# Performance work log

Hardware: AMD Instinct MI355X
Metric: run time of the kernel (lower is better)

The kernel has to match this reference:

```python
import jax, jax.numpy as jnp
import numpy as np

T = 32        # time_step
H = 64        # n_hidden (and dense width)
A = 8         # nb_actions
OBS_DIM = 512
B = 4096      # sequences; obs rows = B*T
LN_EPS = 1e-12  # tf.contrib.layers.layer_norm epsilon


def setup_inputs() -> dict:
    key = jax.random.key(0)
    ks = jax.random.split(key, 10)
    s = 0.1
    return {
        "obs":  jax.random.normal(ks[0], (B * T, OBS_DIM), jnp.float32),
        "W0":   jax.random.normal(ks[1], (OBS_DIM, H), jnp.float32) * s,
        "b0":   jnp.zeros((H,), jnp.float32),
        "gamma": jnp.ones((H,), jnp.float32),
        "beta":  jnp.zeros((H,), jnp.float32),
        "Wfw":  jax.random.normal(ks[2], (2 * H, 4 * H), jnp.float32) * s,
        "bfw":  jnp.zeros((4 * H,), jnp.float32),
        "Wbw":  jax.random.normal(ks[3], (2 * H, 4 * H), jnp.float32) * s,
        "bbw":  jnp.zeros((4 * H,), jnp.float32),
        "Wc":   jax.random.uniform(ks[4], (H, A), jnp.float32, -0.003, 0.003),
        "bc":   jnp.zeros((A,), jnp.float32),
    }


def _lstm_scan(xs, W, b):
    """BasicLSTMCell (forget_bias=1.0). xs: [T, B, H] -> hs: [T, B, H]."""
    nb = xs.shape[1]
    init = (jnp.zeros((nb, H), xs.dtype), jnp.zeros((nb, H), xs.dtype))

    def step(carry, x_t):
        c, h = carry
        z = jnp.concatenate([x_t, h], axis=-1) @ W + b  # [B, 4H]
        i, j, f, o = jnp.split(z, 4, axis=-1)           # TF gate order i,j,f,o
        c = c * jax.nn.sigmoid(f + 1.0) + jax.nn.sigmoid(i) * jnp.tanh(j)
        h = jnp.tanh(c) * jax.nn.sigmoid(o)
        return (c, h), h

    _, hs = jax.lax.scan(step, init, xs)
    return hs


def reference(obs, W0, b0, gamma, beta, Wfw, bfw, Wbw, bbw, Wc, bc):
    # dense(64) + layer_norm + relu
    x = obs @ W0 + b0                                   # [B*T, H]
    mu = jnp.mean(x, axis=-1, keepdims=True)
    var = jnp.mean(jnp.square(x - mu), axis=-1, keepdims=True)
    x = gamma * (x - mu) / jnp.sqrt(var + LN_EPS) + beta
    x = jax.nn.relu(x)

    xt = x.reshape(-1, T, H).transpose(1, 0, 2)          # [T, B, H]
    hs_fw = _lstm_scan(xt, Wfw, bfw)                     # [T, B, H]
    hs_bw = _lstm_scan(xt[::-1], Wbw, bbw)[::-1]         # reverse-in, reverse-out

    # tf.reshape on the (fw, bw) tuple stacks along a new leading axis:
    # [2, B, T, H] -> [2B, T*H, 1]; conv1d(kernel=stride=H) == per-step proj.
    y = jnp.stack([hs_fw.transpose(1, 0, 2), hs_bw.transpose(1, 0, 2)], axis=0)
    y = y.reshape(-1, T, H)                              # [2B, T, H]
    out = jnp.tanh(jnp.einsum('btk,ka->bta', y, Wc) + bc)  # [2B, T, A]
    return out
```

## Files before the change

### kernel.cpp

```cpp
#include <hip/hip_runtime.h>
#include <hip/hip_bf16.h>

typedef __attribute__((ext_vector_type(8))) short bf16x8;
typedef __attribute__((ext_vector_type(4))) float f32x4;

#define MFMA_BF16 __builtin_amdgcn_mfma_f32_16x16x32_bf16

#define GLDS16(gp, lp)                                                        \
  __builtin_amdgcn_global_load_lds(                                           \
      (const __attribute__((address_space(1))) void*)(gp),                    \
      (__attribute__((address_space(3))) void*)(lp), 16, 0, 0)

__device__ __forceinline__ unsigned pk2(float a, float b) {
  __hip_bfloat162 t = __float22bfloat162_rn(make_float2(a, b));
  return *reinterpret_cast<unsigned*>(&t);
}
__device__ __forceinline__ unsigned short f2bf_hw(float f) {
  __hip_bfloat16 h = __float2bfloat16(f);
  return *reinterpret_cast<unsigned short*>(&h);
}

__global__ void k0_conv(const float* __restrict__ W0, const float* __restrict__ Wfw,
                        const float* __restrict__ Wbw, unsigned short* __restrict__ wfrag,
                        unsigned short* __restrict__ wlstm) {
  int gid = blockIdx.x * 256 + threadIdx.x;
  if (gid < 4096) {
    int f = gid >> 6, l = gid & 63;
    int k0 = (f >> 2) * 32 + ((l >> 4) << 3);
    int n = (f & 3) * 16 + (l & 15);
    bf16x8 v;
#pragma unroll
    for (int j = 0; j < 8; ++j) v[j] = (short)f2bf_hw(W0[(k0 + j) * 64 + n]);
    *(bf16x8*)(wfrag + gid * 8) = v;
  } else if (gid < 12288) {
    int g2 = gid - 4096;
    const float* W = (g2 < 4096) ? Wfw : Wbw;
    int f = (g2 & 4095) >> 6, l = g2 & 63;
    int wv = f >> 4, gate = (f >> 2) & 3, kf = f & 3;
    int col = gate * 64 + wv * 16 + (l & 15);
    int kr = kf * 32 + ((l >> 4) << 3);
    bf16x8 v;
#pragma unroll
    for (int j = 0; j < 8; ++j) v[j] = (short)f2bf_hw(W[(kr + j) * 256 + col]);
    *(bf16x8*)(wlstm + g2 * 8) = v;
  }
}

__global__ __launch_bounds__(256, 3) void k_dense_ln(
    const float* __restrict__ obs, const unsigned short* __restrict__ wfrag,
    const float* __restrict__ b0, const float* __restrict__ gam,
    const float* __restrict__ bet, unsigned short* __restrict__ xout) {
  __shared__ __align__(16) char lds[49152];
  const int tid = threadIdx.x, w = tid >> 6, l = tid & 63;
  const int g = l >> 4, c = l & 15;
  const long blk64 = (long)blockIdx.x * 64;
  const long rb = blk64 + w * 16;

  float b0v[4], gv[4], bv[4];
#pragma unroll
  for (int nt = 0; nt < 4; ++nt) {
    int col = nt * 16 + c;
    b0v[nt] = b0[col]; gv[nt] = gam[col]; bv[nt] = bet[col];
  }
  const unsigned short* wfl = wfrag + l * 8;
  const char* gB = (const char*)obs + blk64 * 2048;

  const int rlo = w * 4 + g;
  asm volatile("s_waitcnt vmcnt(0)" ::: "memory");

#define K1_STAGE(q)                                                           \
  {                                                                           \
    _Pragma("unroll") for (int i = 0; i < 4; ++i) {                           \
      int row_ = i * 16 + rlo;                                                \
      const char* gp_ = gB + (long)row_ * 2048 + (q) * 256 +                  \
                        (long)((c ^ rlo) * 16);                               \
      char* lp_ = lds + ((q) % 3) * 16384 + (i * 4096 + (w * 64 + l) * 16);   \
      GLDS16(gp_, lp_);                                                       \
    }                                                                         \
  }

  K1_STAGE(0);
  K1_STAGE(1);
  K1_STAGE(2);

  f32x4 acc[4];
#pragma unroll
  for (int nt = 0; nt < 4; ++nt) acc[nt] = (f32x4){0.f, 0.f, 0.f, 0.f};

#pragma unroll
  for (int q = 0; q < 8; ++q) {
    constexpr int VW[8] = {8, 16, 24, 24, 24, 24, 20, 16};
    asm volatile("s_waitcnt vmcnt(%0)" :: "i"(VW[q]) : "memory");
    __builtin_amdgcn_s_barrier();
    __builtin_amdgcn_sched_barrier(0);

    const char* rowb = lds + (q % 3) * 16384 + (w * 16 + c) * 256;
#pragma unroll
    for (int kf = 0; kf < 2; ++kf) {
      int fb = (q * 2 + kf) * 4;
      bf16x8 B0 = *(const bf16x8*)(wfl + (fb + 0) * 512);
      bf16x8 B1 = *(const bf16x8*)(wfl + (fb + 1) * 512);
      bf16x8 B2 = *(const bf16x8*)(wfl + (fb + 2) * 512);
      bf16x8 B3 = *(const bf16x8*)(wfl + (fb + 3) * 512);
      int u0 = kf * 8 + g * 2;
      float4 f0 = *(const float4*)(rowb + ((u0 + 0) ^ c) * 16);
      float4 f1 = *(const float4*)(rowb + ((u0 + 1) ^ c) * 16);
      union { bf16x8 v; unsigned u[4]; } af;
      af.u[0] = pk2(f0.x, f0.y); af.u[1] = pk2(f0.z, f0.w);
      af.u[2] = pk2(f1.x, f1.y); af.u[3] = pk2(f1.z, f1.w);
      acc[0] = MFMA_BF16(af.v, B0, acc[0], 0, 0, 0);
      acc[1] = MFMA_BF16(af.v, B1, acc[1], 0, 0, 0);
      acc[2] = MFMA_BF16(af.v, B2, acc[2], 0, 0, 0);
      acc[3] = MFMA_BF16(af.v, B3, acc[3], 0, 0, 0);
    }
    if (q < 5) {
      __builtin_amdgcn_s_barrier();
      __builtin_amdgcn_sched_barrier(0);
      K1_STAGE(q + 3);
    }
  }

  float vv[4][4], s1[4], s2[4];
#pragma unroll
  for (int r = 0; r < 4; ++r) { s1[r] = 0.f; s2[r] = 0.f; }
#pragma unroll
  for (int nt = 0; nt < 4; ++nt)
#pragma unroll
    for (int r = 0; r < 4; ++r) {
      float val = acc[nt][r] + b0v[nt];
      vv[nt][r] = val; s1[r] += val; s2[r] += val * val;
    }
#pragma unroll
  for (int r = 0; r < 4; ++r) {
#pragma unroll
    for (int m = 1; m <= 8; m <<= 1) {
      s1[r] += __shfl_xor(s1[r], m);
      s2[r] += __shfl_xor(s2[r], m);
    }
  }
  unsigned short* xw = (unsigned short*)lds + w * 1024;
#pragma unroll
  for (int r = 0; r < 4; ++r) {
    float mu = s1[r] * 0.015625f;
    float var = s2[r] * 0.015625f - mu * mu;
    float inv = rsqrtf(var + 1e-12f);
    int row = g * 4 + r;
#pragma unroll
    for (int nt = 0; nt < 4; ++nt) {
      float xn = (vv[nt][r] - mu) * inv * gv[nt] + bv[nt];
      xw[(row * 64 + nt * 16 + c) ^ (g << 3)] = f2bf_hw(fmaxf(xn, 0.f));
    }
  }
#pragma unroll
  for (int m2 = 0; m2 < 2; ++m2) {
    int m = m2 * 64 + l;
    int row = m >> 3, u8 = m & 7;
    bf16x8 v = *(const bf16x8*)(xw + ((row * 64 + u8 * 8) ^ ((row >> 2) << 3)));
    *(bf16x8*)(xout + (rb + row) * 64 + u8 * 8) = v;
  }
}

__global__ __launch_bounds__(256, 2) void k_lstm(
    const unsigned short* __restrict__ x, const unsigned short* __restrict__ wlstm,
    const float* __restrict__ bfw, const float* __restrict__ bbw,
    const float* __restrict__ Wc, const float* __restrict__ bc,
    float* __restrict__ out) {
  __shared__ __align__(16) char xl[65536];
  __shared__ unsigned short hl[2 * 1024];
  const int tid = threadIdx.x, w = tid >> 6, l = tid & 63;
  const int g = l >> 4, c = l & 15;
  const int dir = blockIdx.x >> 8;
  const int sq = (blockIdx.x & 255) * 16;
  const float* bias = dir ? bbw : bfw;

  bf16x8 Bf[4][4];
  const unsigned short* wl = wlstm + ((long)dir * 4096 + w * 16 * 64) * 8;
#pragma unroll
  for (int gate = 0; gate < 4; ++gate)
#pragma unroll
    for (int kf = 0; kf < 4; ++kf)
      Bf[gate][kf] = *(const bf16x8*)(wl + ((gate * 4 + kf) * 64 + l) * 8);
  float bz[4];
#pragma unroll
  for (int gate = 0; gate < 4; ++gate) bz[gate] = bias[gate * 64 + w * 16 + c];

  bf16x8 Pc[2];
#pragma unroll
  for (int kf = 0; kf < 2; ++kf)
#pragma unroll
    for (int j = 0; j < 8; ++j) Pc[kf][j] = 0;
  float bcv = 0.f;
  if (w == 0 && c < 8) {
#pragma unroll
    for (int kf = 0; kf < 2; ++kf)
#pragma unroll
      for (int j = 0; j < 8; ++j)
        Pc[kf][j] = (short)f2bf_hw(Wc[(kf * 32 + g * 8 + j) * 8 + c]);
    bcv = bc[c];
  }

  asm volatile("s_waitcnt vmcnt(0)" ::: "memory");

  const int ss = l >> 3, sc = l & 7;
#pragma unroll
  for (int j = 0; j < 8; ++j) {
    int tt = w * 8 + j;
    int te = dir ? 31 - tt : tt;
#pragma unroll
    for (int p = 0; p < 2; ++p) {
      int s = p * 8 + ss;
      const char* gp = (const char*)x +
          ((long)(sq + s) * 32 + te) * 128 + (long)(sc ^ (s & 7)) * 16;
      char* lp = xl + tt * 2048 + p * 1024;
      GLDS16(gp, lp);
    }
  }

  for (int i = tid; i < 1024; i += 256) ((unsigned*)hl)[i] = 0u;
  float cs[4] = {0.f, 0.f, 0.f, 0.f};

  if (w == 0) asm volatile("s_waitcnt vmcnt(12)" ::: "memory");
  asm volatile("s_waitcnt lgkmcnt(0)" ::: "memory");
  __builtin_amdgcn_s_barrier();
  __builtin_amdgcn_sched_barrier(0);

  const int hq = w >> 1;
  const int hgp = ((w & 1) * 2 + (c >> 3)) * 16;
  const int hlo = c & 7;

  f32x4 accx[4];
  {
    const char* xt = xl + 0 * 2048 + c * 128;
    bf16x8 Ax0 = *(const bf16x8*)(xt + (long)((g) ^ (c & 7)) * 16);
    bf16x8 Ax1 = *(const bf16x8*)(xt + (long)((4 + g) ^ (c & 7)) * 16);
#pragma unroll
    for (int gate = 0; gate < 4; ++gate) {
      f32x4 b = (f32x4){bz[gate], bz[gate], bz[gate], bz[gate]};
      accx[gate] = MFMA_BF16(Ax1, Bf[gate][1],
                             MFMA_BF16(Ax0, Bf[gate][0], b, 0, 0, 0), 0, 0, 0);
    }
  }

  int p = 0;
#pragma unroll
  for (int t = 0; t < 32; ++t) {
    bf16x8 Ah0 = *(const bf16x8*)((const char*)hl + p * 2048 + l * 16);
    bf16x8 Ah1 = *(const bf16x8*)((const char*)hl + p * 2048 + 1024 + l * 16);

    f32x4 acc[4];
#pragma unroll
    for (int gate = 0; gate < 4; ++gate)
      acc[gate] = MFMA_BF16(Ah1, Bf[gate][3],
                            MFMA_BF16(Ah0, Bf[gate][2], accx[gate], 0, 0, 0),
                            0, 0, 0);

    if (t + 1 < 32) {
      const char* xt = xl + (t + 1) * 2048 + c * 128;
      bf16x8 Ax0 = *(const bf16x8*)(xt + (long)((g) ^ (c & 7)) * 16);
      bf16x8 Ax1 = *(const bf16x8*)(xt + (long)((4 + g) ^ (c & 7)) * 16);
#pragma unroll
      for (int gate = 0; gate < 4; ++gate) {
        f32x4 b = (f32x4){bz[gate], bz[gate], bz[gate], bz[gate]};
        accx[gate] = MFMA_BF16(Ax1, Bf[gate][1],
                               MFMA_BF16(Ax0, Bf[gate][0], b, 0, 0, 0), 0, 0, 0);
      }
    }

    const int wb = (p ^ 1) * 1024;
#pragma unroll
    for (int r = 0; r < 4; ++r) {
      float ei = __expf(-acc[0][r]);
      float ej = __expf(2.f * acc[1][r]);
      float ef = __expf(-(acc[2][r] + 1.f));
      float eo = __expf(-acc[3][r]);
      float p12 = (1.f + ei) * (1.f + ej);
      float r3 = __builtin_amdgcn_rcpf(p12 * (1.f + ef));
      float it = (ej - 1.f) * (1.f + ef) * r3;
      float sf = p12 * r3;
      cs[r] = cs[r] * sf + it;
      float ec = __expf(2.f * cs[r]);
      float r2 = __builtin_amdgcn_rcpf((1.f + eo) * (1.f + ec));
      hl[wb + (hq * 64 + hgp + 4 * g + r) * 8 + hlo] =
          f2bf_hw((ec - 1.f) * r2);
    }

    if (t + 2 < 32) {
      if (w == ((t + 2) >> 3))
        asm volatile("s_waitcnt vmcnt(%0)" :: "i"(14 - 2 * ((t + 2) & 7)) : "memory");
    }
    asm volatile("s_waitcnt lgkmcnt(0)" ::: "memory");
    __builtin_amdgcn_s_barrier();
    __builtin_amdgcn_sched_barrier(0);

    if (w == 0 && t >= 1) {
      int te = dir ? 31 - t : t;
      f32x4 pa = (f32x4){0.f, 0.f, 0.f, 0.f};
      pa = MFMA_BF16(Ah0, Pc[0], pa, 0, 0, 0);
      pa = MFMA_BF16(Ah1, Pc[1], pa, 0, 0, 0);
      if (c < 8) {
        int tp = dir ? 32 - t : t - 1;
#pragma unroll
        for (int r = 0; r < 4; ++r) {
          long orow = (long)dir * 4096 + sq + 4 * g + r;
          out[(orow * 32 + tp) * 8 + c] = tanhf(pa[r] + bcv);
        }
      }
    }
    p ^= 1;
  }

  if (w == 0) {
    bf16x8 Ph0 = *(const bf16x8*)((const char*)hl + p * 2048 + l * 16);
    bf16x8 Ph1 = *(const bf16x8*)((const char*)hl + p * 2048 + 1024 + l * 16);
    f32x4 pa = (f32x4){0.f, 0.f, 0.f, 0.f};
    pa = MFMA_BF16(Ph0, Pc[0], pa, 0, 0, 0);
    pa = MFMA_BF16(Ph1, Pc[1], pa, 0, 0, 0);
    if (c < 8) {
      int tp = dir ? 0 : 31;
#pragma unroll
      for (int r = 0; r < 4; ++r) {
        long orow = (long)dir * 4096 + sq + 4 * g + r;
        out[(orow * 32 + tp) * 8 + c] = tanhf(pa[r] + bcv);
      }
    }
  }
}

extern "C" void kernel_launch(void* const* d_in, const int* in_sizes, int n_in,
                              void* d_out, int out_size, void* d_ws, size_t ws_size,
                              hipStream_t stream) {
  const float* obs = (const float*)d_in[0];
  const float* W0  = (const float*)d_in[1];
  const float* b0  = (const float*)d_in[2];
  const float* gam = (const float*)d_in[3];
  const float* bet = (const float*)d_in[4];
  const float* Wfw = (const float*)d_in[5];
  const float* bfw = (const float*)d_in[6];
  const float* Wbw = (const float*)d_in[7];
  const float* bbw = (const float*)d_in[8];
  const float* Wc  = (const float*)d_in[9];
  const float* bc  = (const float*)d_in[10];
  float* out = (float*)d_out;

  unsigned short* wfrag = (unsigned short*)d_ws;
  unsigned short* wlstm = wfrag + 4096 * 8;
  unsigned short* xbf   = wlstm + 8192 * 8;

  k0_conv<<<48, 256, 0, stream>>>(W0, Wfw, Wbw, wfrag, wlstm);
  k_dense_ln<<<2048, 256, 0, stream>>>(obs, wfrag, b0, gam, bet, xbf);
  k_lstm<<<512, 256, 0, stream>>>(xbf, wlstm, bfw, bbw, Wc, bc, out);
}
```

Measured before the change: 102.3 us.

## Restructure dense-LN loading and spread LSTM output projection across waves

The dense+layernorm kernel now uses 128-thread blocks where each wave loads its entire 16-row obs tile into a private 32KB LDS region up front, instead of running a 3-stage block-wide pipeline with barriers. The MFMA loop double-buffers the weight fragments in registers. In the LSTM kernel, the per-timestep output projection is split across all four waves, replacing the previous wave-0-only work. Staggered vmcnt waits are replaced by a single full wait, partial unrolling is used, and tanhf is replaced with an exp/rcp form. The trade-off is that loads no longer overlap compute within a wave, the LSTM kernel has a longer startup stall, and tanh precision is slightly lower.

```diff
diff --git a/kernel.cpp b/kernel.cpp
--- a/kernel.cpp
+++ b/kernel.cpp
@@ -18,6 +18,9 @@
 __device__ __forceinline__ unsigned short f2bf_hw(float f) {
   __hip_bfloat16 h = __float2bfloat16(f);
   return *reinterpret_cast<unsigned short*>(&h);
+}
+__device__ __forceinline__ float tanh_f(float x) {
+  return 1.f - 2.f * __builtin_amdgcn_rcpf(1.f + __expf(2.f * x));
 }
 
 __global__ void k0_conv(const float* __restrict__ W0, const float* __restrict__ Wfw,
@@ -46,15 +49,15 @@
   }
 }
 
-__global__ __launch_bounds__(256, 3) void k_dense_ln(
+__global__ __launch_bounds__(128) void k_dense_ln(
     const float* __restrict__ obs, const unsigned short* __restrict__ wfrag,
     const float* __restrict__ b0, const float* __restrict__ gam,
     const float* __restrict__ bet, unsigned short* __restrict__ xout) {
-  __shared__ __align__(16) char lds[49152];
+  __shared__ __align__(16) char lds[65536];
   const int tid = threadIdx.x, w = tid >> 6, l = tid & 63;
   const int g = l >> 4, c = l & 15;
-  const long blk64 = (long)blockIdx.x * 64;
-  const long rb = blk64 + w * 16;
+  const long rw = (long)blockIdx.x * 32 + w * 16;
+  char* ldw = lds + w * 32768;
 
   float b0v[4], gv[4], bv[4];
 #pragma unroll
@@ -63,60 +66,50 @@
     b0v[nt] = b0[col]; gv[nt] = gam[col]; bv[nt] = bet[col];
   }
   const unsigned short* wfl = wfrag + l * 8;
-  const char* gB = (const char*)obs + blk64 * 2048;
-
-  const int rlo = w * 4 + g;
+  const char* gW = (const char*)obs + rw * 2048;
+
   asm volatile("s_waitcnt vmcnt(0)" ::: "memory");
 
-#define K1_STAGE(q)                                                           \
-  {                                                                           \
-    _Pragma("unroll") for (int i = 0; i < 4; ++i) {                           \
-      int row_ = i * 16 + rlo;                                                \
-      const char* gp_ = gB + (long)row_ * 2048 + (q) * 256 +                  \
-                        (long)((c ^ rlo) * 16);                               \
-      char* lp_ = lds + ((q) % 3) * 16384 + (i * 4096 + (w * 64 + l) * 16);   \
-      GLDS16(gp_, lp_);                                                       \
-    }                                                                         \
-  }
-
-  K1_STAGE(0);
-  K1_STAGE(1);
-  K1_STAGE(2);
+#pragma unroll
+  for (int i = 0; i < 32; ++i) {
+    int ri = i >> 1, hi = i & 1;
+    const char* gp = gW + ri * 2048 + hi * 1024 + (long)((l ^ (ri & 7)) * 16);
+    char* lp = ldw + ri * 2048 + hi * 1024;
+    GLDS16(gp, lp);
+  }
+  asm volatile("s_waitcnt vmcnt(0)" ::: "memory");
+  __builtin_amdgcn_sched_barrier(0);
 
   f32x4 acc[4];
 #pragma unroll
   for (int nt = 0; nt < 4; ++nt) acc[nt] = (f32x4){0.f, 0.f, 0.f, 0.f};
 
-#pragma unroll
-  for (int q = 0; q < 8; ++q) {
-    constexpr int VW[8] = {8, 16, 24, 24, 24, 24, 20, 16};
-    asm volatile("s_waitcnt vmcnt(%0)" :: "i"(VW[q]) : "memory");
-    __builtin_amdgcn_s_barrier();
-    __builtin_amdgcn_sched_barrier(0);
-
-    const char* rowb = lds + (q % 3) * 16384 + (w * 16 + c) * 256;
-#pragma unroll
-    for (int kf = 0; kf < 2; ++kf) {
-      int fb = (q * 2 + kf) * 4;
-      bf16x8 B0 = *(const bf16x8*)(wfl + (fb + 0) * 512);
-      bf16x8 B1 = *(const bf16x8*)(wfl + (fb + 1) * 512);
-      bf16x8 B2 = *(const bf16x8*)(wfl + (fb + 2) * 512);
-      bf16x8 B3 = *(const bf16x8*)(wfl + (fb + 3) * 512);
-      int u0 = kf * 8 + g * 2;
-      float4 f0 = *(const float4*)(rowb + ((u0 + 0) ^ c) * 16);
-      float4 f1 = *(const float4*)(rowb + ((u0 + 1) ^ c) * 16);
-      union { bf16x8 v; unsigned u[4]; } af;
-      af.u[0] = pk2(f0.x, f0.y); af.u[1] = pk2(f0.z, f0.w);
-      af.u[2] = pk2(f1.x, f1.y); af.u[3] = pk2(f1.z, f1.w);
-      acc[0] = MFMA_BF16(af.v, B0, acc[0], 0, 0, 0);
-      acc[1] = MFMA_BF16(af.v, B1, acc[1], 0, 0, 0);
-      acc[2] = MFMA_BF16(af.v, B2, acc[2], 0, 0, 0);
-      acc[3] = MFMA_BF16(af.v, B3, acc[3], 0, 0, 0);
-    }
-    if (q < 5) {
-      __builtin_amdgcn_s_barrier();
-      __builtin_amdgcn_sched_barrier(0);
-      K1_STAGE(q + 3);
+  const char* rowb = ldw + c * 2048;
+  bf16x8 Bc[4];
+#pragma unroll
+  for (int nt = 0; nt < 4; ++nt) Bc[nt] = *(const bf16x8*)(wfl + nt * 512);
+
+#pragma unroll
+  for (int kf = 0; kf < 16; ++kf) {
+    int s0 = kf * 8 + g * 2;
+    float4 f0 = *(const float4*)(rowb + (long)((s0 ^ (c & 7)) * 16));
+    float4 f1 = *(const float4*)(rowb + (long)(((s0 + 1) ^ (c & 7)) * 16));
+    bf16x8 Bn[4];
+    if (kf < 15) {
+#pragma unroll
+      for (int nt = 0; nt < 4; ++nt)
+        Bn[nt] = *(const bf16x8*)(wfl + ((kf + 1) * 4 + nt) * 512);
+    }
+    union { bf16x8 v; unsigned u[4]; } af;
+    af.u[0] = pk2(f0.x, f0.y); af.u[1] = pk2(f0.z, f0.w);
+    af.u[2] = pk2(f1.x, f1.y); af.u[3] = pk2(f1.z, f1.w);
+    acc[0] = MFMA_BF16(af.v, Bc[0], acc[0], 0, 0, 0);
+    acc[1] = MFMA_BF16(af.v, Bc[1], acc[1], 0, 0, 0);
+    acc[2] = MFMA_BF16(af.v, Bc[2], acc[2], 0, 0, 0);
+    acc[3] = MFMA_BF16(af.v, Bc[3], acc[3], 0, 0, 0);
+    if (kf < 15) {
+#pragma unroll
+      for (int nt = 0; nt < 4; ++nt) Bc[nt] = Bn[nt];
     }
   }
 
@@ -138,7 +131,7 @@
       s2[r] += __shfl_xor(s2[r], m);
     }
   }
-  unsigned short* xw = (unsigned short*)lds + w * 1024;
+  unsigned short* xw = (unsigned short*)ldw;
 #pragma unroll
   for (int r = 0; r < 4; ++r) {
     float mu = s1[r] * 0.015625f;
@@ -156,7 +149,7 @@
     int m = m2 * 64 + l;
     int row = m >> 3, u8 = m & 7;
     bf16x8 v = *(const bf16x8*)(xw + ((row * 64 + u8 * 8) ^ ((row >> 2) << 3)));
-    *(bf16x8*)(xout + (rb + row) * 64 + u8 * 8) = v;
+    *(bf16x8*)(xout + (rw + row) * 64 + u8 * 8) = v;
   }
 }
 
@@ -190,7 +183,7 @@
 #pragma unroll
     for (int j = 0; j < 8; ++j) Pc[kf][j] = 0;
   float bcv = 0.f;
-  if (w == 0 && c < 8) {
+  if (c < 8) {
 #pragma unroll
     for (int kf = 0; kf < 2; ++kf)
 #pragma unroll
@@ -219,7 +212,7 @@
   for (int i = tid; i < 1024; i += 256) ((unsigned*)hl)[i] = 0u;
   float cs[4] = {0.f, 0.f, 0.f, 0.f};
 
-  if (w == 0) asm volatile("s_waitcnt vmcnt(12)" ::: "memory");
+  asm volatile("s_waitcnt vmcnt(0)" ::: "memory");
   asm volatile("s_waitcnt lgkmcnt(0)" ::: "memory");
   __builtin_amdgcn_s_barrier();
   __builtin_amdgcn_sched_barrier(0);
@@ -230,7 +223,7 @@
 
   f32x4 accx[4];
   {
-    const char* xt = xl + 0 * 2048 + c * 128;
+    const char* xt = xl + c * 128;
     bf16x8 Ax0 = *(const bf16x8*)(xt + (long)((g) ^ (c & 7)) * 16);
     bf16x8 Ax1 = *(const bf16x8*)(xt + (long)((4 + g) ^ (c & 7)) * 16);
 #pragma unroll
@@ -242,7 +235,7 @@
   }
 
   int p = 0;
-#pragma unroll
+#pragma unroll 2
   for (int t = 0; t < 32; ++t) {
     bf16x8 Ah0 = *(const bf16x8*)((const char*)hl + p * 2048 + l * 16);
     bf16x8 Ah1 = *(const bf16x8*)((const char*)hl + p * 2048 + 1024 + l * 16);
@@ -280,47 +273,41 @@
       cs[r] = cs[r] * sf + it;
       float ec = __expf(2.f * cs[r]);
       float r2 = __builtin_amdgcn_rcpf((1.f + eo) * (1.f + ec));
-      hl[wb + (hq * 64 + hgp + 4 * g + r) * 8 + hlo] =
-          f2bf_hw((ec - 1.f) * r2);
-    }
-
-    if (t + 2 < 32) {
-      if (w == ((t + 2) >> 3))
-        asm volatile("s_waitcnt vmcnt(%0)" :: "i"(14 - 2 * ((t + 2) & 7)) : "memory");
-    }
+      hl[wb + (hq * 64 + hgp + 4 * g + r) * 8 + hlo] = f2bf_hw((ec - 1.f) * r2);
+    }
+
     asm volatile("s_waitcnt lgkmcnt(0)" ::: "memory");
     __builtin_amdgcn_s_barrier();
     __builtin_amdgcn_sched_barrier(0);
 
-    if (w == 0 && t >= 1) {
-      int te = dir ? 31 - t : t;
+    if (t >= 1) {
       f32x4 pa = (f32x4){0.f, 0.f, 0.f, 0.f};
       pa = MFMA_BF16(Ah0, Pc[0], pa, 0, 0, 0);
       pa = MFMA_BF16(Ah1, Pc[1], pa, 0, 0, 0);
-      if (c < 8) {
+      if (g == w && c < 8) {
         int tp = dir ? 32 - t : t - 1;
 #pragma unroll
         for (int r = 0; r < 4; ++r) {
           long orow = (long)dir * 4096 + sq + 4 * g + r;
-          out[(orow * 32 + tp) * 8 + c] = tanhf(pa[r] + bcv);
+          out[(orow * 32 + tp) * 8 + c] = tanh_f(pa[r] + bcv);
         }
       }
     }
     p ^= 1;
   }
 
-  if (w == 0) {
+  {
     bf16x8 Ph0 = *(const bf16x8*)((const char*)hl + p * 2048 + l * 16);
     bf16x8 Ph1 = *(const bf16x8*)((const char*)hl + p * 2048 + 1024 + l * 16);
     f32x4 pa = (f32x4){0.f, 0.f, 0.f, 0.f};
     pa = MFMA_BF16(Ph0, Pc[0], pa, 0, 0, 0);
     pa = MFMA_BF16(Ph1, Pc[1], pa, 0, 0, 0);
-    if (c < 8) {
+    if (g == w && c < 8) {
       int tp = dir ? 0 : 31;
 #pragma unroll
       for (int r = 0; r < 4; ++r) {
         long orow = (long)dir * 4096 + sq + 4 * g + r;
-        out[(orow * 32 + tp) * 8 + c] = tanhf(pa[r] + bcv);
+        out[(orow * 32 + tp) * 8 + c] = tanh_f(pa[r] + bcv);
       }
     }
   }
@@ -347,6 +334,6 @@
   unsigned short* xbf   = wlstm + 8192 * 8;
 
   k0_conv<<<48, 256, 0, stream>>>(W0, Wfw, Wbw, wfrag, wlstm);
-  k_dense_ln<<<2048, 256, 0, stream>>>(obs, wfrag, b0, gam, bet, xbf);
+  k_dense_ln<<<4096, 128, 0, stream>>>(obs, wfrag, b0, gam, bet, xbf);
   k_lstm<<<512, 256, 0, stream>>>(xbf, wlstm, bfw, bbw, Wc, bc, out);
 }
```

New measurement: 128.1 us. 25.3% more time.
